# Performance work log

Hardware: AMD Instinct MI355X
Metric: run time of the kernel (lower is better)

## Reference

```python
import jax, jax.numpy as jnp
import numpy as np

N_VISIBLE = 4096
N_HIDDEN = 4096
BATCH = 8192


def setup_inputs() -> dict:
    key = jax.random.key(0)
    k_x, k_w = jax.random.split(key)
    input_data = jax.random.uniform(k_x, (BATCH, N_VISIBLE), dtype=jnp.float32)
    # xavier_uniform with sigmoid gain (=1.0): limit = sqrt(6/(fan_in+fan_out))
    limit = float(np.sqrt(6.0 / (N_VISIBLE + N_HIDDEN)))
    W = jax.random.uniform(k_w, (N_VISIBLE, N_HIDDEN), dtype=jnp.float32,
                           minval=-limit, maxval=limit)
    hidden_bias = jnp.zeros((N_HIDDEN,), dtype=jnp.float32)
    return {"input_data": input_data, "W": W, "hidden_bias": hidden_bias}


def reference(input_data, W, hidden_bias):
    # RBM.sample_hidden_2 (forward): sigmoid(x @ W + b), batched over samples.
    # (The torch code loops per sample with host syncs; same math, vectorized.)
    hid_prob = jax.nn.sigmoid(jnp.matmul(input_data, W) + hidden_bias)
    return hid_prob
```

## Files before the change

kernel.cpp:

```cpp
#include <hip/hip_runtime.h>
#include <cstdint>

#define MDIM 8192
#define NDIM 4096
#define KDIM 4096
#define NT (KDIM / 64)

typedef __bf16 bf16x8 __attribute__((ext_vector_type(8)));
typedef float f32x4 __attribute__((ext_vector_type(4)));

#define MFMA16 __builtin_amdgcn_mfma_f32_16x16x32_bf16

__device__ __forceinline__ void gload_lds16(const void* g, void* l) {
    __builtin_amdgcn_global_load_lds(
        (const __attribute__((address_space(1))) uint32_t*)g,
        (__attribute__((address_space(3))) uint32_t*)l, 16, 0, 0);
}

__device__ __forceinline__ unsigned short bf16_bits(float f) {
    __bf16 b = (__bf16)f;
    return __builtin_bit_cast(unsigned short, b);
}

__device__ __forceinline__ int detect_f32(const void* X) {
    int ok = 1;
    if (threadIdx.x < 128) {
        unsigned short h = ((const unsigned short*)X)[threadIdx.x];
        ok = (h <= 0x3F80);
    }
    return __syncthreads_and(ok) ? 0 : 1;
}

__global__ __launch_bounds__(256) void prep(const void* __restrict__ X,
                                            const void* __restrict__ W,
                                            __bf16* __restrict__ Xb,
                                            __bf16* __restrict__ WT) {
    const int f32 = detect_f32(X);
    const int t = threadIdx.x;
    if (blockIdx.x < 8192) {
        if (!f32) return;
        const float* Xf = (const float*)X;
        const long xbase = (long)blockIdx.x * 4096;
#pragma unroll
        for (int rr = 0; rr < 4; ++rr) {
            const long idx = xbase + rr * 1024 + t * 4;
            float4 v = *(const float4*)(Xf + idx);
            unsigned short r[4] = {bf16_bits(v.x), bf16_bits(v.y),
                                   bf16_bits(v.z), bf16_bits(v.w)};
            *(uint2*)(Xb + idx) = *(const uint2*)r;
        }
        return;
    }
    __shared__ unsigned short tile[64 * 65];
    const int bid = blockIdx.x - 8192;
    const int n0 = (bid & 63) * 64;
    const int k0 = (bid >> 6) * 64;
    if (f32) {
        const float* Wf = (const float*)W;
#pragma unroll
        for (int p = 0; p < 4; ++p) {
            const int ch = p * 256 + t;
            const int kr = ch >> 4;
            const int nc = ch & 15;
            float4 v = *(const float4*)(Wf + (long)(k0 + kr) * NDIM + n0 + nc * 4);
            tile[(nc * 4 + 0) * 65 + kr] = bf16_bits(v.x);
            tile[(nc * 4 + 1) * 65 + kr] = bf16_bits(v.y);
            tile[(nc * 4 + 2) * 65 + kr] = bf16_bits(v.z);
            tile[(nc * 4 + 3) * 65 + kr] = bf16_bits(v.w);
        }
    } else {
        const __bf16* Wb = (const __bf16*)W;
#pragma unroll
        for (int p = 0; p < 2; ++p) {
            const int ch = p * 256 + t;
            const int kr = ch >> 3;
            const int nc = ch & 7;
            uint4 v = *(const uint4*)(Wb + (long)(k0 + kr) * NDIM + n0 + nc * 8);
            const unsigned short* e = (const unsigned short*)&v;
#pragma unroll
            for (int i = 0; i < 8; ++i) tile[(nc * 8 + i) * 65 + kr] = e[i];
        }
    }
    __syncthreads();
#pragma unroll
    for (int p = 0; p < 2; ++p) {
        const int ch = p * 256 + t;
        const int nr = ch >> 3;
        const int kc = ch & 7;
        unsigned short r[8];
#pragma unroll
        for (int i = 0; i < 8; ++i) r[i] = tile[nr * 65 + kc * 8 + i];
        *(uint4*)(WT + (long)(n0 + nr) * KDIM + k0 + kc * 8) = *(uint4*)r;
    }
}

__global__ __launch_bounds__(256) void transpose_w(const void* __restrict__ X,
                                                   const void* __restrict__ W,
                                                   __bf16* __restrict__ WT) {
    __shared__ unsigned short tile[64 * 65];
    const int f32 = detect_f32(X);
    const int t = threadIdx.x;
    const int k0 = blockIdx.y * 64;
    const int n0 = blockIdx.x * 64;
    if (f32) {
        const float* Wf = (const float*)W;
#pragma unroll
        for (int p = 0; p < 4; ++p) {
            const int ch = p * 256 + t;
            const int kr = ch >> 4;
            const int nc = ch & 15;
            float4 v = *(const float4*)(Wf + (long)(k0 + kr) * NDIM + n0 + nc * 4);
            tile[(nc * 4 + 0) * 65 + kr] = bf16_bits(v.x);
            tile[(nc * 4 + 1) * 65 + kr] = bf16_bits(v.y);
            tile[(nc * 4 + 2) * 65 + kr] = bf16_bits(v.z);
            tile[(nc * 4 + 3) * 65 + kr] = bf16_bits(v.w);
        }
    } else {
        const __bf16* Wb = (const __bf16*)W;
#pragma unroll
        for (int p = 0; p < 2; ++p) {
            const int ch = p * 256 + t;
            const int kr = ch >> 3;
            const int nc = ch & 7;
            uint4 v = *(const uint4*)(Wb + (long)(k0 + kr) * NDIM + n0 + nc * 8);
            const unsigned short* e = (const unsigned short*)&v;
#pragma unroll
            for (int i = 0; i < 8; ++i) tile[(nc * 8 + i) * 65 + kr] = e[i];
        }
    }
    __syncthreads();
#pragma unroll
    for (int p = 0; p < 2; ++p) {
        const int ch = p * 256 + t;
        const int nr = ch >> 3;
        const int kc = ch & 7;
        unsigned short r[8];
#pragma unroll
        for (int i = 0; i < 8; ++i) r[i] = tile[nr * 65 + kc * 8 + i];
        *(uint4*)(WT + (long)(n0 + nr) * KDIM + k0 + kc * 8) = *(uint4*)r;
    }
}

#define P_OPEN()                                           \
    do {                                                   \
        __builtin_amdgcn_sched_barrier(0);                 \
        __builtin_amdgcn_s_barrier();                      \
        asm volatile("s_waitcnt lgkmcnt(0)" ::: "memory"); \
        __builtin_amdgcn_sched_barrier(0);                 \
    } while (0)
#define P_CLOSE()                          \
    do {                                   \
        __builtin_amdgcn_sched_barrier(0); \
        __builtin_amdgcn_s_barrier();      \
    } while (0)

#define CL(Q)                                                                \
    do {                                                                     \
        __builtin_amdgcn_s_setprio(1);                                       \
        _Pragma("unroll") for (int kk = 0; kk < 2; ++kk)                     \
            _Pragma("unroll") for (int ii = 0; ii < 2; ++ii)                 \
                _Pragma("unroll") for (int j = 0; j < 4; ++j)                \
                    acc[2 * (Q) + ii][j] = MFMA16(aF[ii][kk], bF[j][kk],     \
                                                  acc[2 * (Q) + ii][j], 0, 0, 0); \
        __builtin_amdgcn_s_setprio(0);                                       \
    } while (0)

#define READ_AQ(OFF)                                          \
    do {                                                      \
        aF[0][0] = *(const bf16x8*)(paT + (OFF) + soff0);     \
        aF[0][1] = *(const bf16x8*)(paT + (OFF) + soff1);     \
        aF[1][0] = *(const bf16x8*)(paT + (OFF) + 1024 + soff0); \
        aF[1][1] = *(const bf16x8*)(paT + (OFF) + 1024 + soff1); \
    } while (0)

template <int DB>
__device__ __forceinline__ void ktile(const __bf16* pa, const __bf16* pb,
                                      const __bf16* gA, const __bf16* gB,
                                      __bf16* lA, __bf16* lB,
                                      long ko1, long ko2,
                                      int soff0, int soff1,
                                      f32x4 (&acc)[8][4]) {
    const __bf16* paT = pa + DB * 16384;
    const __bf16* pbT = pb + DB * 16384;
    bf16x8 aF[2][2], bF[4][2];
#pragma unroll
    for (int j = 0; j < 4; ++j) {
        bF[j][0] = *(const bf16x8*)(pbT + j * 1024 + soff0);
        bF[j][1] = *(const bf16x8*)(pbT + j * 1024 + soff1);
    }
    READ_AQ(0);
    gload_lds16(gA + (long)128 * KDIM + ko1, lA + (DB ^ 1) * 16384 + 8192);
    gload_lds16(gA + (long)192 * KDIM + ko1, lA + (DB ^ 1) * 16384 + 12288);
    asm volatile("s_waitcnt lgkmcnt(8)" ::: "memory");
    P_OPEN();
    CL(0);
    P_CLOSE();
    READ_AQ(2048);
    gload_lds16(gB + ko2, lB + DB * 16384);
    gload_lds16(gB + (long)64 * KDIM + ko2, lB + DB * 16384 + 4096);
    P_OPEN();
    CL(1);
    P_CLOSE();
    READ_AQ(8192);
    gload_lds16(gA + ko2, lA + DB * 16384);
    gload_lds16(gA + (long)64 * KDIM + ko2, lA + DB * 16384 + 4096);
    P_OPEN();
    CL(2);
    P_CLOSE();
    READ_AQ(10240);
    gload_lds16(gB + (long)128 * KDIM + ko2, lB + DB * 16384 + 8192);
    gload_lds16(gB + (long)192 * KDIM + ko2, lB + DB * 16384 + 12288);
    P_OPEN();
    CL(3);
    __builtin_amdgcn_sched_barrier(0);
    asm volatile("s_waitcnt vmcnt(6)" ::: "memory");
    __builtin_amdgcn_sched_barrier(0);
    __builtin_amdgcn_s_barrier();
}

__global__ __launch_bounds__(512, 2) void gemm256(
    const void* __restrict__ X, const __bf16* __restrict__ Xb,
    const __bf16* __restrict__ WT, const void* __restrict__ bias,
    void* __restrict__ out) {
    __shared__ __bf16 sA[2][256][64];
    __shared__ __bf16 sB[2][256][64];
    const int f32 = detect_f32(X);
    const __bf16* __restrict__ Abf = f32 ? Xb : (const __bf16*)X;
    const int t = threadIdx.x;
    const int lane = t & 63;
    const int wid = t >> 6;
    const int wm = wid >> 2;
    const int wn = wid & 3;
    const int lrow = lane & 15;
    const int quad = lane >> 4;
    const int l7 = lrow & 7;

    const int flat = blockIdx.x;
    const int swz = (flat & 7) * (512 / 8) + (flat >> 3);
    const long m0 = (long)(swz >> 4) * 256;
    const long n0 = (long)(swz & 15) * 256;

    const int r8 = lane >> 3;
    const int c8 = lane & 7;
    const int cs = (c8 ^ r8) * 8;
    const __bf16* gA = Abf + (m0 + wid * 8 + r8) * KDIM + cs;
    const __bf16* gB = WT + (n0 + wid * 8 + r8) * KDIM + cs;
    __bf16* lA = &sA[0][wid * 8][0];
    __bf16* lB = &sB[0][wid * 8][0];

    const int soff0 = (quad ^ l7) * 8;
    const int soff1 = ((4 + quad) ^ l7) * 8;
    const __bf16* pa = &sA[0][wm * 64 + lrow][0];
    const __bf16* pb = &sB[0][wn * 64 + lrow][0];

    f32x4 acc[8][4] = {};

    gload_lds16(gB, lB);
    gload_lds16(gB + (long)64 * KDIM, lB + 4096);
    gload_lds16(gA, lA);
    gload_lds16(gA + (long)64 * KDIM, lA + 4096);
    gload_lds16(gB + (long)128 * KDIM, lB + 8192);
    gload_lds16(gB + (long)192 * KDIM, lB + 12288);
    gload_lds16(gA + (long)128 * KDIM, lA + 8192);
    gload_lds16(gA + (long)192 * KDIM, lA + 12288);
    gload_lds16(gB + 64, lB + 16384);
    gload_lds16(gB + (long)64 * KDIM + 64, lB + 16384 + 4096);
    gload_lds16(gA + 64, lA + 16384);
    gload_lds16(gA + (long)64 * KDIM + 64, lA + 16384 + 4096);
    gload_lds16(gB + (long)128 * KDIM + 64, lB + 16384 + 8192);
    gload_lds16(gB + (long)192 * KDIM + 64, lB + 16384 + 12288);
    __builtin_amdgcn_sched_barrier(0);
    asm volatile("s_waitcnt vmcnt(6)" ::: "memory");
    __builtin_amdgcn_sched_barrier(0);
    __builtin_amdgcn_s_barrier();

#pragma unroll 1
    for (int tt = 0; tt < NT; tt += 2) {
        ktile<0>(pa, pb, gA, gB, lA, lB, (long)((tt + 1) & (NT - 1)) * 64,
                 (long)((tt + 2) & (NT - 1)) * 64, soff0, soff1, acc);
        ktile<1>(pa, pb, gA, gB, lA, lB, (long)((tt + 2) & (NT - 1)) * 64,
                 (long)((tt + 3) & (NT - 1)) * 64, soff0, soff1, acc);
    }

    if (f32) {
        float* of = (float*)out;
        const float* bf = (const float*)bias;
#pragma unroll
        for (int j = 0; j < 4; ++j) {
            const int col = (int)n0 + wn * 64 + j * 16 + lrow;
            const float bv = bf[col];
#pragma unroll
            for (int i = 0; i < 8; ++i) {
                const int rr = (int)m0 + (i >> 2) * 128 + wm * 64 +
                               (i & 3) * 16 + quad * 4;
                const long rbase = (long)rr * NDIM + col;
#pragma unroll
                for (int r = 0; r < 4; ++r) {
                    const float x = acc[i][j][r] + bv;
                    of[rbase + (long)r * NDIM] = 1.0f / (1.0f + __expf(-x));
                }
            }
        }
    } else {
        __bf16* ob = (__bf16*)out;
        const __bf16* bb = (const __bf16*)bias;
#pragma unroll
        for (int j = 0; j < 4; ++j) {
            const int col = (int)n0 + wn * 64 + j * 16 + lrow;
            const float bv = (float)bb[col];
#pragma unroll
            for (int i = 0; i < 8; ++i) {
                const int rr = (int)m0 + (i >> 2) * 128 + wm * 64 +
                               (i & 3) * 16 + quad * 4;
                const long rbase = (long)rr * NDIM + col;
#pragma unroll
                for (int r = 0; r < 4; ++r) {
                    const float x = acc[i][j][r] + bv;
                    ob[rbase + (long)r * NDIM] = (__bf16)(1.0f / (1.0f + __expf(-x)));
                }
            }
        }
    }
}

template <int MODE>
__global__ __launch_bounds__(256) void gemm_bias_sigmoid(
    const void* __restrict__ X, const __bf16* __restrict__ Xb,
    const void* __restrict__ Wp, const __bf16* __restrict__ WT,
    const void* __restrict__ bias, void* __restrict__ out) {
    __shared__ __bf16 sA[128 * 64];
    __shared__ __bf16 sB[128 * 64];
    const int f32 = detect_f32(X);
    const int t = threadIdx.x;
    const int lane = t & 63;
    const int wid = t >> 6;
    const int m0 = blockIdx.y * 128;
    const int n0 = blockIdx.x * 128;
    const int wm = (wid & 1) * 64;
    const int wn = (wid >> 1) * 64;
    const int lrow = lane & 15;
    const int quad = lane >> 4;

    f32x4 acc[4][4] = {};

    {
        const int srow = t >> 2;
        const int schk = t & 3;
        __bf16* ldsA = sA + wid * 512;
        __bf16* ldsB = sB + wid * 512;
        const int arow = t >> 1;
        const int acol = (t & 1) * 16;
        const int fp = t & 15;
        const int fc = t >> 4;
        uint32_t* sB32 = (uint32_t*)sB;

        auto compute = [&]() {
            bf16x8 aF[4], bFr[4];
            const __bf16* pa = sA + (wm + lrow) * 32 + quad * 8;
            const __bf16* pb = sB + (wn + lrow) * 32 + quad * 8;
#pragma unroll
            for (int i = 0; i < 4; ++i) aF[i] = *(const bf16x8*)(pa + i * 512);
#pragma unroll
            for (int j = 0; j < 4; ++j) bFr[j] = *(const bf16x8*)(pb + j * 512);
#pragma unroll
            for (int i = 0; i < 4; ++i)
#pragma unroll
                for (int j = 0; j < 4; ++j)
                    acc[i][j] = MFMA16(aF[i], bFr[j], acc[i][j], 0, 0, 0);
        };

        if (MODE == 1 && !f32) {
            const __bf16* gA = (const __bf16*)X + (long)(m0 + srow) * KDIM + schk * 8;
            const __bf16* gB = WT + (long)(n0 + srow) * KDIM + schk * 8;
            for (int kt = 0; kt < KDIM / 32; ++kt) {
                const __bf16* a0 = gA + kt * 32;
                gload_lds16(a0, ldsA);
                gload_lds16(a0 + (long)64 * KDIM, ldsA + 2048);
                const __bf16* b0 = gB + kt * 32;
                gload_lds16(b0, ldsB);
                gload_lds16(b0 + (long)64 * KDIM, ldsB + 2048);
                __syncthreads();
                compute();
                __syncthreads();
            }
        } else if (MODE == 1) {
            const float* Xf = (const float*)X;
            const __bf16* gB = WT + (long)(n0 + srow) * KDIM + schk * 8;
            for (int kt = 0; kt < KDIM / 32; ++kt) {
                const __bf16* b0 = gB + kt * 32;
                gload_lds16(b0, ldsB);
                gload_lds16(b0 + (long)64 * KDIM, ldsB + 2048);
                const float* ap = Xf + (long)(m0 + arow) * KDIM + kt * 32 + acol;
                float4 v0 = *(const float4*)(ap);
                float4 v1 = *(const float4*)(ap + 4);
                float4 v2 = *(const float4*)(ap + 8);
                float4 v3 = *(const float4*)(ap + 12);
                unsigned short r[16] = {
                    bf16_bits(v0.x), bf16_bits(v0.y), bf16_bits(v0.z), bf16_bits(v0.w),
                    bf16_bits(v1.x), bf16_bits(v1.y), bf16_bits(v1.z), bf16_bits(v1.w),
                    bf16_bits(v2.x), bf16_bits(v2.y), bf16_bits(v2.z), bf16_bits(v2.w),
                    bf16_bits(v3.x), bf16_bits(v3.y), bf16_bits(v3.z), bf16_bits(v3.w)};
                *(uint4*)(sA + arow * 32 + acol) = *(const uint4*)(r);
                *(uint4*)(sA + arow * 32 + acol + 8) = *(const uint4*)(r + 8);
                __syncthreads();
                compute();
                __syncthreads();
            }
        } else if (MODE == 2 && !f32) {
            const __bf16* gA = (const __bf16*)X + (long)(m0 + srow) * KDIM + schk * 8;
            const __bf16* Wb = (const __bf16*)Wp;
            for (int kt = 0; kt < KDIM / 32; ++kt) {
                const __bf16* a0 = gA + kt * 32;
                gload_lds16(a0, ldsA);
                gload_lds16(a0 + (long)64 * KDIM, ldsA + 2048);
                const __bf16* w0 = Wb + (long)(kt * 32 + 2 * fp) * NDIM + n0 + fc * 8;
                uint4 g0 = *(const uint4*)(w0);
                uint4 g1 = *(const uint4*)(w0 + NDIM);
                const unsigned short* e0 = (const unsigned short*)&g0;
                const unsigned short* e1 = (const unsigned short*)&g1;
#pragma unroll
                for (int i = 0; i < 8; ++i)
                    sB32[(fc * 8 + i) * 16 + fp] =
                        (uint32_t)e0[i] | ((uint32_t)e1[i] << 16);
                __syncthreads();
                compute();
                __syncthreads();
            }
        } else if (MODE == 2) {
            const float* Xf = (const float*)X;
            const float* Wf = (const float*)Wp;
            for (int kt = 0; kt < KDIM / 32; ++kt) {
                const float* ap = Xf + (long)(m0 + arow) * KDIM + kt * 32 + acol;
                float4 v0 = *(const float4*)(ap);
                float4 v1 = *(const float4*)(ap + 4);
                float4 v2 = *(const float4*)(ap + 8);
                float4 v3 = *(const float4*)(ap + 12);
                unsigned short r[16] = {
                    bf16_bits(v0.x), bf16_bits(v0.y), bf16_bits(v0.z), bf16_bits(v0.w),
                    bf16_bits(v1.x), bf16_bits(v1.y), bf16_bits(v1.z), bf16_bits(v1.w),
                    bf16_bits(v2.x), bf16_bits(v2.y), bf16_bits(v2.z), bf16_bits(v2.w),
                    bf16_bits(v3.x), bf16_bits(v3.y), bf16_bits(v3.z), bf16_bits(v3.w)};
                *(uint4*)(sA + arow * 32 + acol) = *(const uint4*)(r);
                *(uint4*)(sA + arow * 32 + acol + 8) = *(const uint4*)(r + 8);
                const float* w0 = Wf + (long)(kt * 32 + 2 * fp) * NDIM + n0 + fc * 8;
                float4 u0 = *(const float4*)(w0);
                float4 u1 = *(const float4*)(w0 + 4);
                float4 u2 = *(const float4*)(w0 + NDIM);
                float4 u3 = *(const float4*)(w0 + NDIM + 4);
                float k0v[8] = {u0.x, u0.y, u0.z, u0.w, u1.x, u1.y, u1.z, u1.w};
                float k1v[8] = {u2.x, u2.y, u2.z, u2.w, u3.x, u3.y, u3.z, u3.w};
#pragma unroll
                for (int i = 0; i < 8; ++i)
                    sB32[(fc * 8 + i) * 16 + fp] =
                        (uint32_t)bf16_bits(k0v[i]) |
                        ((uint32_t)bf16_bits(k1v[i]) << 16);
                __syncthreads();
                compute();
                __syncthreads();
            }
        }
    }

    const int crow = m0 + wm + quad * 4;
    if (f32) {
        float* of = (float*)out;
        const float* bf = (const float*)bias;
#pragma unroll
        for (int j = 0; j < 4; ++j) {
            const int col = n0 + wn + j * 16 + lrow;
            const float bv = bf[col];
#pragma unroll
            for (int i = 0; i < 4; ++i) {
                const long rbase = (long)(crow + i * 16) * NDIM + col;
#pragma unroll
                for (int r = 0; r < 4; ++r) {
                    const float x = acc[i][j][r] + bv;
                    of[rbase + (long)r * NDIM] = 1.0f / (1.0f + __expf(-x));
                }
            }
        }
    } else {
        __bf16* ob = (__bf16*)out;
        const __bf16* bb = (const __bf16*)bias;
#pragma unroll
        for (int j = 0; j < 4; ++j) {
            const int col = n0 + wn + j * 16 + lrow;
            const float bv = (float)bb[col];
#pragma unroll
            for (int i = 0; i < 4; ++i) {
                const long rbase = (long)(crow + i * 16) * NDIM + col;
#pragma unroll
                for (int r = 0; r < 4; ++r) {
                    const float x = acc[i][j][r] + bv;
                    ob[rbase + (long)r * NDIM] = (__bf16)(1.0f / (1.0f + __expf(-x)));
                }
            }
        }
    }
}

extern "C" void kernel_launch(void* const* d_in, const int* in_sizes, int n_in,
                              void* d_out, int out_size, void* d_ws,
                              size_t ws_size, hipStream_t stream) {
    const void* X = d_in[0];
    const void* W = d_in[1];
    const void* bias = d_in[2];

    const size_t wt_bytes = (size_t)KDIM * NDIM * sizeof(__bf16);
    const size_t xb_bytes = (size_t)MDIM * KDIM * sizeof(__bf16);

    if (ws_size >= wt_bytes + xb_bytes) {
        __bf16* WT = (__bf16*)d_ws;
        __bf16* Xb = (__bf16*)((char*)d_ws + wt_bytes);
        prep<<<8192 + 4096, 256, 0, stream>>>(X, W, Xb, WT);
        gemm256<<<dim3((MDIM / 256) * (NDIM / 256)), 512, 0, stream>>>(
            X, Xb, WT, bias, d_out);
    } else if (ws_size >= wt_bytes) {
        __bf16* WT = (__bf16*)d_ws;
        transpose_w<<<dim3(NDIM / 64, KDIM / 64), 256, 0, stream>>>(X, W, WT);
        dim3 gg(NDIM / 128, MDIM / 128);
        gemm_bias_sigmoid<1><<<gg, 256, 0, stream>>>(X, nullptr, W, WT, bias, d_out);
    } else {
        dim3 gg(NDIM / 128, MDIM / 128);
        gemm_bias_sigmoid<2><<<gg, 256, 0, stream>>>(X, nullptr, W, nullptr, bias, d_out);
    }
}
```

Baseline: 527.4 us.

## Use 4 waves with 128x128 warp tiles and register-double-buffered B fragments

Reworks the 256x256 GEMM tile from 8 waves each computing 128x64 to 4 waves each computing 128x128, with B fragments double-buffered in registers across k-tiles. All global-to-LDS loads for the next k-tile are issued at the start of each tile, replacing the interleaved 4-phase schedule that used per-phase barriers. The goal is fewer LDS reads per MFMA and fewer barriers, at the cost of much higher register pressure (256 accumulator floats per lane), launch_bounds changing to one 256-thread block per unit, and reduced latency hiding from fewer waves.

```diff
diff --git a/kernel.cpp b/kernel.cpp
--- a/kernel.cpp
+++ b/kernel.cpp
@@ -10,6 +10,7 @@
 typedef float f32x4 __attribute__((ext_vector_type(4)));
 
 #define MFMA16 __builtin_amdgcn_mfma_f32_16x16x32_bf16
+#define SB0 __builtin_amdgcn_sched_barrier(0)
 
 __device__ __forceinline__ void gload_lds16(const void* g, void* l) {
     __builtin_amdgcn_global_load_lds(
@@ -141,84 +142,113 @@
     }
 }
 
-#define P_OPEN()                                           \
-    do {                                                   \
-        __builtin_amdgcn_sched_barrier(0);                 \
-        __builtin_amdgcn_s_barrier();                      \
-        asm volatile("s_waitcnt lgkmcnt(0)" ::: "memory"); \
-        __builtin_amdgcn_sched_barrier(0);                 \
+#define WAITL(N)                                                \
+    do {                                                        \
+        SB0;                                                    \
+        asm volatile("s_waitcnt lgkmcnt(" #N ")" ::: "memory"); \
+        SB0;                                                    \
     } while (0)
-#define P_CLOSE()                          \
-    do {                                   \
-        __builtin_amdgcn_sched_barrier(0); \
-        __builtin_amdgcn_s_barrier();      \
+
+#define CLW(c)                                                              \
+    do {                                                                    \
+        _Pragma("unroll") for (int kk = 0; kk < 2; ++kk)                    \
+            _Pragma("unroll") for (int j = 0; j < 8; ++j)                   \
+                acc[c][j] = MFMA16(Aw[(c) & 1][kk], Bc[j][kk], acc[c][j],   \
+                                   0, 0, 0);                                \
     } while (0)
 
-#define CL(Q)                                                                \
-    do {                                                                     \
-        __builtin_amdgcn_s_setprio(1);                                       \
-        _Pragma("unroll") for (int kk = 0; kk < 2; ++kk)                     \
-            _Pragma("unroll") for (int ii = 0; ii < 2; ++ii)                 \
-                _Pragma("unroll") for (int j = 0; j < 4; ++j)                \
-                    acc[2 * (Q) + ii][j] = MFMA16(aF[ii][kk], bF[j][kk],     \
-                                                  acc[2 * (Q) + ii][j], 0, 0, 0); \
-        __builtin_amdgcn_s_setprio(0);                                       \
+#define ISS_A(p, base, fi)                                       \
+    do {                                                         \
+        Aw[p][0] = *(const bf16x8*)((base) + (fi)*1024 + soff0); \
+        Aw[p][1] = *(const bf16x8*)((base) + (fi)*1024 + soff1); \
     } while (0)
 
-#define READ_AQ(OFF)                                          \
-    do {                                                      \
-        aF[0][0] = *(const bf16x8*)(paT + (OFF) + soff0);     \
-        aF[0][1] = *(const bf16x8*)(paT + (OFF) + soff1);     \
-        aF[1][0] = *(const bf16x8*)(paT + (OFF) + 1024 + soff0); \
-        aF[1][1] = *(const bf16x8*)(paT + (OFF) + 1024 + soff1); \
+#define ISS_B2(j0, base)                                                 \
+    do {                                                                 \
+        Bn[(j0)][0] = *(const bf16x8*)((base) + (j0)*1024 + soff0);      \
+        Bn[(j0)][1] = *(const bf16x8*)((base) + (j0)*1024 + soff1);      \
+        Bn[(j0) + 1][0] =                                                \
+            *(const bf16x8*)((base) + ((j0) + 1) * 1024 + soff0);        \
+        Bn[(j0) + 1][1] =                                                \
+            *(const bf16x8*)((base) + ((j0) + 1) * 1024 + soff1);        \
     } while (0)
 
 template <int DB>
 __device__ __forceinline__ void ktile(const __bf16* pa, const __bf16* pb,
                                       const __bf16* gA, const __bf16* gB,
-                                      __bf16* lA, __bf16* lB,
-                                      long ko1, long ko2,
-                                      int soff0, int soff1,
-                                      f32x4 (&acc)[8][4]) {
+                                      __bf16* lA, __bf16* lB, long ko1,
+                                      int soff0, int soff1, f32x4 (&acc)[8][8],
+                                      bf16x8 (&Bc)[8][2], bf16x8 (&Bn)[8][2],
+                                      bf16x8 (&Aw)[2][2]) {
     const __bf16* paT = pa + DB * 16384;
-    const __bf16* pbT = pb + DB * 16384;
-    bf16x8 aF[2][2], bF[4][2];
-#pragma unroll
-    for (int j = 0; j < 4; ++j) {
-        bF[j][0] = *(const bf16x8*)(pbT + j * 1024 + soff0);
-        bF[j][1] = *(const bf16x8*)(pbT + j * 1024 + soff1);
-    }
-    READ_AQ(0);
-    gload_lds16(gA + (long)128 * KDIM + ko1, lA + (DB ^ 1) * 16384 + 8192);
-    gload_lds16(gA + (long)192 * KDIM + ko1, lA + (DB ^ 1) * 16384 + 12288);
-    asm volatile("s_waitcnt lgkmcnt(8)" ::: "memory");
-    P_OPEN();
-    CL(0);
-    P_CLOSE();
-    READ_AQ(2048);
-    gload_lds16(gB + ko2, lB + DB * 16384);
-    gload_lds16(gB + (long)64 * KDIM + ko2, lB + DB * 16384 + 4096);
-    P_OPEN();
-    CL(1);
-    P_CLOSE();
-    READ_AQ(8192);
-    gload_lds16(gA + ko2, lA + DB * 16384);
-    gload_lds16(gA + (long)64 * KDIM + ko2, lA + DB * 16384 + 4096);
-    P_OPEN();
-    CL(2);
-    P_CLOSE();
-    READ_AQ(10240);
-    gload_lds16(gB + (long)128 * KDIM + ko2, lB + DB * 16384 + 8192);
-    gload_lds16(gB + (long)192 * KDIM + ko2, lB + DB * 16384 + 12288);
-    P_OPEN();
-    CL(3);
-    __builtin_amdgcn_sched_barrier(0);
-    asm volatile("s_waitcnt vmcnt(6)" ::: "memory");
-    __builtin_amdgcn_sched_barrier(0);
+    const __bf16* paN = pa + (DB ^ 1) * 16384;
+    const __bf16* pbN = pb + (DB ^ 1) * 16384;
+    const int so = (DB ^ 1) * 16384;
+    SB0;
     __builtin_amdgcn_s_barrier();
-}
-
-__global__ __launch_bounds__(512, 2) void gemm256(
+    SB0;
+#pragma unroll
+    for (int i = 0; i < 8; ++i)
+        gload_lds16(gA + (long)(i * 32) * KDIM + ko1, lA + so + i * 2048);
+#pragma unroll
+    for (int i = 0; i < 8; ++i)
+        gload_lds16(gB + (long)(i * 32) * KDIM + ko1, lB + so + i * 2048);
+    SB0;
+    WAITL(0);
+    CLW(0);
+    SB0;
+    ISS_A(1, paT, 1);
+    SB0;
+    WAITL(0);
+    CLW(1);
+    SB0;
+    ISS_A(0, paT, 2);
+    SB0;
+    WAITL(0);
+    CLW(2);
+    SB0;
+    ISS_A(1, paT, 3);
+    SB0;
+    WAITL(0);
+    CLW(3);
+    SB0;
+    ISS_A(0, paT, 4);
+    SB0;
+    asm volatile("s_waitcnt vmcnt(0)" ::: "memory");
+    SB0;
+    __builtin_amdgcn_s_barrier();
+    SB0;
+    WAITL(0);
+    CLW(4);
+    SB0;
+    ISS_A(1, paT, 5);
+    SB0;
+    ISS_B2(0, pbN);
+    SB0;
+    WAITL(4);
+    CLW(5);
+    SB0;
+    ISS_A(0, paT, 6);
+    SB0;
+    ISS_B2(2, pbN);
+    SB0;
+    WAITL(4);
+    CLW(6);
+    SB0;
+    ISS_A(1, paT, 7);
+    SB0;
+    ISS_B2(4, pbN);
+    SB0;
+    WAITL(4);
+    CLW(7);
+    SB0;
+    ISS_A(0, paN, 0);
+    SB0;
+    ISS_B2(6, pbN);
+    SB0;
+}
+
+__global__ __launch_bounds__(256, 1) void gemm256(
     const void* __restrict__ X, const __bf16* __restrict__ Xb,
     const __bf16* __restrict__ WT, const void* __restrict__ bias,
     void* __restrict__ out) {
@@ -229,8 +259,8 @@
     const int t = threadIdx.x;
     const int lane = t & 63;
     const int wid = t >> 6;
-    const int wm = wid >> 2;
-    const int wn = wid & 3;
+    const int wm = wid >> 1;
+    const int wn = wid & 1;
     const int lrow = lane & 15;
     const int quad = lane >> 4;
     const int l7 = lrow & 7;
@@ -250,49 +280,50 @@
 
     const int soff0 = (quad ^ l7) * 8;
     const int soff1 = ((4 + quad) ^ l7) * 8;
-    const __bf16* pa = &sA[0][wm * 64 + lrow][0];
-    const __bf16* pb = &sB[0][wn * 64 + lrow][0];
-
-    f32x4 acc[8][4] = {};
-
-    gload_lds16(gB, lB);
-    gload_lds16(gB + (long)64 * KDIM, lB + 4096);
-    gload_lds16(gA, lA);
-    gload_lds16(gA + (long)64 * KDIM, lA + 4096);
-    gload_lds16(gB + (long)128 * KDIM, lB + 8192);
-    gload_lds16(gB + (long)192 * KDIM, lB + 12288);
-    gload_lds16(gA + (long)128 * KDIM, lA + 8192);
-    gload_lds16(gA + (long)192 * KDIM, lA + 12288);
-    gload_lds16(gB + 64, lB + 16384);
-    gload_lds16(gB + (long)64 * KDIM + 64, lB + 16384 + 4096);
-    gload_lds16(gA + 64, lA + 16384);
-    gload_lds16(gA + (long)64 * KDIM + 64, lA + 16384 + 4096);
-    gload_lds16(gB + (long)128 * KDIM + 64, lB + 16384 + 8192);
-    gload_lds16(gB + (long)192 * KDIM + 64, lB + 16384 + 12288);
-    __builtin_amdgcn_sched_barrier(0);
-    asm volatile("s_waitcnt vmcnt(6)" ::: "memory");
-    __builtin_amdgcn_sched_barrier(0);
+    const __bf16* pa = &sA[0][wm * 128 + lrow][0];
+    const __bf16* pb = &sB[0][wn * 128 + lrow][0];
+
+    f32x4 acc[8][8] = {};
+    bf16x8 Ba[8][2], Bb[8][2], Aw[2][2];
+
+#pragma unroll
+    for (int i = 0; i < 8; ++i)
+        gload_lds16(gA + (long)(i * 32) * KDIM, lA + i * 2048);
+#pragma unroll
+    for (int i = 0; i < 8; ++i)
+        gload_lds16(gB + (long)(i * 32) * KDIM, lB + i * 2048);
+    SB0;
+    asm volatile("s_waitcnt vmcnt(0)" ::: "memory");
+    SB0;
     __builtin_amdgcn_s_barrier();
+    SB0;
+#pragma unroll
+    for (int j = 0; j < 8; ++j) {
+        Ba[j][0] = *(const bf16x8*)(pb + j * 1024 + soff0);
+        Ba[j][1] = *(const bf16x8*)(pb + j * 1024 + soff1);
+    }
+    Aw[0][0] = *(const bf16x8*)(pa + soff0);
+    Aw[0][1] = *(const bf16x8*)(pa + soff1);
+    SB0;
 
 #pragma unroll 1
     for (int tt = 0; tt < NT; tt += 2) {
         ktile<0>(pa, pb, gA, gB, lA, lB, (long)((tt + 1) & (NT - 1)) * 64,
-                 (long)((tt + 2) & (NT - 1)) * 64, soff0, soff1, acc);
+                 soff0, soff1, acc, Ba, Bb, Aw);
         ktile<1>(pa, pb, gA, gB, lA, lB, (long)((tt + 2) & (NT - 1)) * 64,
-                 (long)((tt + 3) & (NT - 1)) * 64, soff0, soff1, acc);
+                 soff0, soff1, acc, Bb, Ba, Aw);
     }
 
     if (f32) {
         float* of = (float*)out;
         const float* bf = (const float*)bias;
 #pragma unroll
-        for (int j = 0; j < 4; ++j) {
-            const int col = (int)n0 + wn * 64 + j * 16 + lrow;
+        for (int j = 0; j < 8; ++j) {
+            const int col = (int)n0 + wn * 128 + j * 16 + lrow;
             const float bv = bf[col];
 #pragma unroll
             for (int i = 0; i < 8; ++i) {
-                const int rr = (int)m0 + (i >> 2) * 128 + wm * 64 +
-                               (i & 3) * 16 + quad * 4;
+                const int rr = (int)m0 + wm * 128 + i * 16 + quad * 4;
                 const long rbase = (long)rr * NDIM + col;
 #pragma unroll
                 for (int r = 0; r < 4; ++r) {
@@ -305,13 +336,12 @@
         __bf16* ob = (__bf16*)out;
         const __bf16* bb = (const __bf16*)bias;
 #pragma unroll
-        for (int j = 0; j < 4; ++j) {
-            const int col = (int)n0 + wn * 64 + j * 16 + lrow;
+        for (int j = 0; j < 8; ++j) {
+            const int col = (int)n0 + wn * 128 + j * 16 + lrow;
             const float bv = (float)bb[col];
 #pragma unroll
             for (int i = 0; i < 8; ++i) {
-                const int rr = (int)m0 + (i >> 2) * 128 + wm * 64 +
-                               (i & 3) * 16 + quad * 4;
+                const int rr = (int)m0 + wm * 128 + i * 16 + quad * 4;
                 const long rbase = (long)rr * NDIM + col;
 #pragma unroll
                 for (int r = 0; r < 4; ++r) {
@@ -513,7 +543,7 @@
         __bf16* WT = (__bf16*)d_ws;
         __bf16* Xb = (__bf16*)((char*)d_ws + wt_bytes);
         prep<<<8192 + 4096, 256, 0, stream>>>(X, W, Xb, WT);
-        gemm256<<<dim3((MDIM / 256) * (NDIM / 256)), 512, 0, stream>>>(
+        gemm256<<<dim3((MDIM / 256) * (NDIM / 256)), 256, 0, stream>>>(
             X, Xb, WT, bias, d_out);
     } else if (ws_size >= wt_bytes) {
         __bf16* WT = (__bf16*)d_ws;
```

New measurement: 1.125 ms. 2.13x slower.
